# Kernel tuning notes

Hardware: AMD Instinct MI355X
Metric: run time of the kernel (lower is better)

## Reference

```python
import jax, jax.numpy as jnp
import numpy as np

D_FEATURE = 1024
HEAD = 16
D_K = 64
D_V = 64
EPS = 1e-6


def setup_inputs() -> dict:
    key = jax.random.key(0)
    ks = jax.random.split(key, 12)
    B, S = 2, 2048
    s_in = 1.0 / np.sqrt(D_FEATURE)
    s_o = 1.0 / np.sqrt(HEAD * D_V)
    return {
        "q": jax.random.normal(ks[0], (B, S, D_FEATURE), jnp.float32),
        "k": jax.random.normal(ks[1], (B, S, D_FEATURE), jnp.float32),
        "v": jax.random.normal(ks[2], (B, S, D_FEATURE), jnp.float32),
        "Wq": jax.random.uniform(ks[3], (D_FEATURE, HEAD * D_K), jnp.float32, -s_in, s_in),
        "bq": jnp.zeros((HEAD * D_K,), jnp.float32),
        "Wk": jax.random.uniform(ks[4], (D_FEATURE, HEAD * D_K), jnp.float32, -s_in, s_in),
        "bk": jnp.zeros((HEAD * D_K,), jnp.float32),
        "Wv": jax.random.uniform(ks[5], (D_FEATURE, HEAD * D_V), jnp.float32, -s_in, s_in),
        "bv": jnp.zeros((HEAD * D_V,), jnp.float32),
        "Wo": jax.random.uniform(ks[6], (HEAD * D_V, D_FEATURE), jnp.float32, -s_o, s_o),
        "bo": jnp.zeros((D_FEATURE,), jnp.float32),
        "gamma": jnp.ones((D_FEATURE,), jnp.float32),
        "beta": jnp.zeros((D_FEATURE,), jnp.float32),
    }


def reference(q, k, v, Wq, bq, Wk, bk, Wv, bv, Wo, bo, gamma, beta):
    B, Sq, _ = q.shape
    Sk, Sv = k.shape[1], v.shape[1]
    shortcut = v
    # projections -> (b, h, s, d)
    qh = (q @ Wq + bq).reshape(B, Sq, HEAD, D_K).transpose(0, 2, 1, 3)
    kh = (k @ Wk + bk).reshape(B, Sk, HEAD, D_K).transpose(0, 2, 1, 3)
    vh = (v @ Wv + bv).reshape(B, Sv, HEAD, D_V).transpose(0, 2, 1, 3)
    scale = 1.0 / np.sqrt(D_K).astype(np.float32)
    scores = jnp.einsum('bhqd,bhkd->bhqk', qh * scale, kh)
    attn = jax.nn.softmax(scores, axis=-1)  # dropout is identity (p=0 / eval)
    ctx = jnp.einsum('bhqk,bhkd->bhqd', attn, vh)
    ctx = ctx.transpose(0, 2, 1, 3).reshape(B, Sv, HEAD * D_V)
    out = ctx @ Wo + bo
    out = out + shortcut
    # LayerNorm, eps=1e-6
    mu = out.mean(-1, keepdims=True)
    var = out.var(-1, keepdims=True)
    out = (out - mu) * jax.lax.rsqrt(var + EPS) * gamma + beta
    return out
```

## Files before the change

kernel.cpp:

```cpp
#include <hip/hip_runtime.h>

#define D_FEAT 1024
#define NTOK   4096
#define SEQ    2048
#define NHEAD  16
#define DK     64
#define SPST   72
#define QSCALE 0.1803368801111204f

typedef float          f32x4 __attribute__((ext_vector_type(4)));
typedef short          s16x8 __attribute__((ext_vector_type(8)));
typedef unsigned short u16x4 __attribute__((ext_vector_type(4)));

__device__ __forceinline__ unsigned short f2bf(float f) {
  union { float f; unsigned int u; } x; x.f = f;
  unsigned int r = x.u + 0x7fffu + ((x.u >> 16) & 1u);
  return (unsigned short)(r >> 16);
}

__device__ __forceinline__ f32x4 mfma16(s16x8 a, s16x8 b, f32x4 c) {
  return __builtin_amdgcn_mfma_f32_16x16x32_bf16(a, b, c, 0, 0, 0);
}

__device__ __forceinline__ void gload16(const void* g, void* l) {
  __builtin_amdgcn_global_load_lds(
      (const __attribute__((address_space(1))) void*)g,
      (__attribute__((address_space(3))) void*)l, 16, 0, 0);
}

__global__ __launch_bounds__(256) void cast_bf16_kernel(
    const float* __restrict__ q, const float* __restrict__ k, const float* __restrict__ v,
    unsigned short* __restrict__ qb, unsigned short* __restrict__ kb, unsigned short* __restrict__ vb)
{
  int sel = blockIdx.y;
  const float* src = sel == 0 ? q : (sel == 1 ? k : v);
  unsigned short* dst = sel == 0 ? qb : (sel == 1 ? kb : vb);
  size_t i = ((size_t)blockIdx.x * 256 + threadIdx.x) * 4;
  float4 f = *(const float4*)(src + i);
  u16x4 o; o.x = f2bf(f.x); o.y = f2bf(f.y); o.z = f2bf(f.z); o.w = f2bf(f.w);
  *(u16x4*)(dst + i) = o;
}

__global__ __launch_bounds__(256) void transpose_cast_kernel(
    const float* __restrict__ W0, const float* __restrict__ W1,
    const float* __restrict__ W2, const float* __restrict__ W3,
    unsigned short* __restrict__ WT, unsigned short* __restrict__ Wot)
{
  __shared__ float tile[32][33];
  int z = blockIdx.z;
  const float* W = z == 0 ? W0 : z == 1 ? W1 : z == 2 ? W2 : W3;
  unsigned short* T = (z < 3) ? (WT + (size_t)z * 1024 * 1024) : Wot;
  int tx = threadIdx.x, ty = threadIdx.y;
  int n = blockIdx.x * 32 + tx;
  for (int i = 0; i < 4; ++i) {
    int k = blockIdx.y * 32 + ty + i * 8;
    tile[ty + i * 8][tx] = W[(size_t)k * D_FEAT + n];
  }
  __syncthreads();
  int k = blockIdx.y * 32 + tx;
  for (int i = 0; i < 4; ++i) {
    int n2 = blockIdx.x * 32 + ty + i * 8;
    T[(size_t)n2 * D_FEAT + k] = f2bf(tile[tx][ty + i * 8]);
  }
}

__global__ __launch_bounds__(256) void gemm_qkv(
    const unsigned short* __restrict__ qb, const unsigned short* __restrict__ kb,
    const unsigned short* __restrict__ vb, const unsigned short* __restrict__ WT,
    const float* __restrict__ bq, const float* __restrict__ bk, const float* __restrict__ bv,
    unsigned short* __restrict__ Qp, unsigned short* __restrict__ Kp, unsigned short* __restrict__ Vt)
{
  __shared__ __align__(16) unsigned short sA[128 * 32];
  __shared__ __align__(16) unsigned short sB[128 * 32];
  const int tid = threadIdx.x;
  const int wave = tid >> 6, lane = tid & 63;
  const int quad = lane >> 4, l16 = lane & 15;
  const int wx = wave & 1, wy = wave >> 1;
  const int bx = blockIdx.x;
  const int chunk = bx >> 3;

  const unsigned short* rA;
  const unsigned short* rB;
  int m0, n0;
  if (chunk < 2) {
    m0 = blockIdx.y * 128; n0 = (bx & 7) * 128;
    rA = (chunk ? kb : qb) + (size_t)m0 * D_FEAT;
    rB = WT + (size_t)(chunk * 1024 + n0) * D_FEAT;
  } else {
    m0 = (bx & 7) * 128; n0 = blockIdx.y * 128;
    rA = WT + (size_t)(2048 + m0) * D_FEAT;
    rB = vb + (size_t)n0 * D_FEAT;
  }

  f32x4 acc[4][4];
  for (int mt = 0; mt < 4; ++mt)
    for (int nt = 0; nt < 4; ++nt) acc[mt][nt] = (f32x4){0.f, 0.f, 0.f, 0.f};

  const int rw = lane >> 2;
  const int cl = (((lane & 3) ^ ((lane >> 3) & 3))) * 8;
  const int g0 = (quad ^ ((l16 >> 1) & 3)) * 8;

  for (int k0 = 0; k0 < D_FEAT; k0 += 32) {
    __syncthreads();
    for (int j = 0; j < 2; ++j) {
      int ch = wave * 2 + j;
      gload16(rA + (size_t)(ch * 16 + rw) * D_FEAT + k0 + cl, sA + ch * 512);
      gload16(rB + (size_t)(ch * 16 + rw) * D_FEAT + k0 + cl, sB + ch * 512);
    }
    __syncthreads();
    s16x8 af[4], bfr[4];
    for (int mt = 0; mt < 4; ++mt)
      af[mt] = *(const s16x8*)(sA + (wy * 64 + mt * 16 + l16) * 32 + g0);
    for (int nt = 0; nt < 4; ++nt)
      bfr[nt] = *(const s16x8*)(sB + (wx * 64 + nt * 16 + l16) * 32 + g0);
    for (int mt = 0; mt < 4; ++mt)
      for (int nt = 0; nt < 4; ++nt)
        acc[mt][nt] = mfma16(af[mt], bfr[nt], acc[mt][nt]);
  }

  if (chunk < 2) {
    const float* bias = chunk ? bk : bq;
    unsigned short* Cp = chunk ? Kp : Qp;
    const float scale = chunk == 0 ? QSCALE : 1.0f;
    for (int mt = 0; mt < 4; ++mt)
      for (int nt = 0; nt < 4; ++nt) {
        int col = n0 + wx * 64 + nt * 16 + l16;
        float bcol = bias[col];
        for (int r = 0; r < 4; ++r) {
          int row = m0 + wy * 64 + mt * 16 + quad * 4 + r;
          Cp[(size_t)row * D_FEAT + col] = f2bf((acc[mt][nt][r] + bcol) * scale);
        }
      }
  } else {
    for (int mt = 0; mt < 4; ++mt) {
      float bfeat[4];
      for (int r = 0; r < 4; ++r)
        bfeat[r] = bv[m0 + wy * 64 + mt * 16 + quad * 4 + r];
      for (int nt = 0; nt < 4; ++nt) {
        int n = n0 + wx * 64 + nt * 16 + l16;
        int b = n >> 11, tok = n & 2047;
        for (int r = 0; r < 4; ++r) {
          int f = m0 + wy * 64 + mt * 16 + quad * 4 + r;
          int h = f >> 6, dv = f & 63;
          Vt[(((size_t)(b * 16 + h) * 64 + dv) * SEQ) + tok] =
              f2bf(acc[mt][nt][r] + bfeat[r]);
        }
      }
    }
  }
}

__global__ __launch_bounds__(256) void gemm_o(
    const unsigned short* __restrict__ A, const unsigned short* __restrict__ Bt,
    const float* __restrict__ bias, const float* __restrict__ resid,
    float* __restrict__ Cout)
{
  __shared__ __align__(16) unsigned short sA[128 * 32];
  __shared__ __align__(16) unsigned short sB[128 * 32];
  const int tid = threadIdx.x;
  const int wave = tid >> 6, lane = tid & 63;
  const int quad = lane >> 4, l16 = lane & 15;
  const int wx = wave & 1, wy = wave >> 1;
  const int n0 = blockIdx.x * 128, m0 = blockIdx.y * 128;

  f32x4 acc[4][4];
  for (int mt = 0; mt < 4; ++mt)
    for (int nt = 0; nt < 4; ++nt) acc[mt][nt] = (f32x4){0.f, 0.f, 0.f, 0.f};

  const int rw = lane >> 2;
  const int cl = (((lane & 3) ^ ((lane >> 3) & 3))) * 8;
  const int g0 = (quad ^ ((l16 >> 1) & 3)) * 8;

  for (int k0 = 0; k0 < D_FEAT; k0 += 32) {
    __syncthreads();
    for (int j = 0; j < 2; ++j) {
      int ch = wave * 2 + j;
      gload16(A + (size_t)(m0 + ch * 16 + rw) * D_FEAT + k0 + cl, sA + ch * 512);
      gload16(Bt + (size_t)(n0 + ch * 16 + rw) * D_FEAT + k0 + cl, sB + ch * 512);
    }
    __syncthreads();
    s16x8 af[4], bfr[4];
    for (int mt = 0; mt < 4; ++mt)
      af[mt] = *(const s16x8*)(sA + (wy * 64 + mt * 16 + l16) * 32 + g0);
    for (int nt = 0; nt < 4; ++nt)
      bfr[nt] = *(const s16x8*)(sB + (wx * 64 + nt * 16 + l16) * 32 + g0);
    for (int mt = 0; mt < 4; ++mt)
      for (int nt = 0; nt < 4; ++nt)
        acc[mt][nt] = mfma16(af[mt], bfr[nt], acc[mt][nt]);
  }

  for (int mt = 0; mt < 4; ++mt)
    for (int nt = 0; nt < 4; ++nt) {
      int col = n0 + wx * 64 + nt * 16 + l16;
      float bcol = bias[col];
      for (int r = 0; r < 4; ++r) {
        int row = m0 + wy * 64 + mt * 16 + quad * 4 + r;
        Cout[(size_t)row * D_FEAT + col] =
            acc[mt][nt][r] + bcol + resid[(size_t)row * D_FEAT + col];
      }
    }
}

__global__ __launch_bounds__(256, 4) void flash_kernel(
    const unsigned short* __restrict__ Qp,
    const unsigned short* __restrict__ Kp,
    const unsigned short* __restrict__ Vt,
    unsigned short* __restrict__ ctx)
{
  __shared__ __align__(16) unsigned short sQ[64 * 64];
  __shared__ __align__(16) unsigned short sK[64 * 64];
  __shared__ __align__(16) unsigned short sV[64 * 64];
  __shared__ __align__(16) unsigned short sP[64 * SPST];

  const int tid = threadIdx.x;
  const int wave = tid >> 6, lane = tid & 63;
  const int quad = lane >> 4, l16 = lane & 15;
  const int q0 = blockIdx.x * 64;
  const int bh = blockIdx.y, b = bh >> 4, h = bh & 15;
  const size_t base = (size_t)b * SEQ * D_FEAT + (size_t)h * DK;
  const unsigned short* vt = Vt + (size_t)bh * 64 * SEQ;

  for (int i = 0; i < 2; ++i) {
    int c = tid + 256 * i;
    int row = c >> 3, csw = ((c & 7) ^ (row & 7)) * 8;
    *(s16x8*)(sQ + row * 64 + csw) =
        *(const s16x8*)(Qp + base + (size_t)(q0 + row) * D_FEAT + (c & 7) * 8);
  }
  __syncthreads();

  const int sw = l16 & 7;
  const int c0 = (quad ^ sw) * 8;
  const int c1 = ((quad + 4) ^ sw) * 8;

  const s16x8 bq0 = *(const s16x8*)(sQ + (wave * 16 + l16) * 64 + c0);
  const s16x8 bq1 = *(const s16x8*)(sQ + (wave * 16 + l16) * 64 + c1);

  s16x8 ones;
  for (int j = 0; j < 8; ++j) ones[j] = (short)0x3F80;

  float m_i = -INFINITY;
  f32x4 l_i = (f32x4){0.f, 0.f, 0.f, 0.f};
  f32x4 o[4];
  for (int nt = 0; nt < 4; ++nt) o[nt] = (f32x4){0.f, 0.f, 0.f, 0.f};

  const int rw = lane >> 3;
  const int cls = ((lane & 7) ^ (lane >> 3)) * 8;

  for (int k0 = 0; k0 < SEQ; k0 += 64) {
    __syncthreads();
    for (int j = 0; j < 2; ++j) {
      int ch = wave * 2 + j;
      gload16(Kp + base + (size_t)(k0 + ch * 8 + rw) * D_FEAT + cls, sK + ch * 512);
      gload16(vt + (size_t)(ch * 8 + rw) * SEQ + k0 + cls, sV + ch * 512);
    }
    __syncthreads();

    f32x4 st[4];
    for (int nt = 0; nt < 4; ++nt) {
      s16x8 ak0 = *(const s16x8*)(sK + (nt * 16 + l16) * 64 + c0);
      s16x8 ak1 = *(const s16x8*)(sK + (nt * 16 + l16) * 64 + c1);
      f32x4 z = (f32x4){0.f, 0.f, 0.f, 0.f};
      z = mfma16(ak0, bq0, z);
      st[nt] = mfma16(ak1, bq1, z);
    }

    float mx = st[0][0];
    for (int nt = 0; nt < 4; ++nt)
      for (int r = 0; r < 4; ++r) mx = fmaxf(mx, st[nt][r]);
    mx = fmaxf(mx, __shfl_xor(mx, 16, 64));
    mx = fmaxf(mx, __shfl_xor(mx, 32, 64));
    float mn = fmaxf(m_i, mx);
    float alpha = __builtin_exp2f(m_i - mn);
    m_i = mn;

    for (int nt = 0; nt < 4; ++nt) {
      unsigned int u[4];
      for (int r = 0; r < 4; ++r) {
        union { float f; unsigned int v; } x;
        x.f = __builtin_exp2f(st[nt][r] - mn);
        u[r] = x.v;
      }
      unsigned int w0 = __builtin_amdgcn_perm(u[1], u[0], 0x07060302u);
      unsigned int w1 = __builtin_amdgcn_perm(u[3], u[2], 0x07060302u);
      *(uint2*)(sP + (wave * 16 + l16) * SPST + nt * 16 + quad * 4) =
          make_uint2(w0, w1);
    }

    float ar[4];
    for (int r = 0; r < 4; ++r) ar[r] = __shfl(alpha, quad * 4 + r, 64);
    for (int nt = 0; nt < 4; ++nt)
      for (int r = 0; r < 4; ++r) o[nt][r] *= ar[r];
    for (int r = 0; r < 4; ++r) l_i[r] *= ar[r];

    s16x8 ap0 = *(const s16x8*)(sP + (wave * 16 + l16) * SPST + quad * 8);
    s16x8 ap1 = *(const s16x8*)(sP + (wave * 16 + l16) * SPST + 32 + quad * 8);

    f32x4 zs = (f32x4){0.f, 0.f, 0.f, 0.f};
    zs = mfma16(ap0, ones, zs);
    zs = mfma16(ap1, ones, zs);
    for (int r = 0; r < 4; ++r) l_i[r] += zs[r];

    for (int nt = 0; nt < 4; ++nt) {
      s16x8 bv0 = *(const s16x8*)(sV + (nt * 16 + l16) * 64 + c0);
      s16x8 bv1 = *(const s16x8*)(sV + (nt * 16 + l16) * 64 + c1);
      o[nt] = mfma16(ap0, bv0, o[nt]);
      o[nt] = mfma16(ap1, bv1, o[nt]);
    }
  }

  float inv[4];
  for (int r = 0; r < 4; ++r) inv[r] = __builtin_amdgcn_rcpf(l_i[r]);
  for (int nt = 0; nt < 4; ++nt)
    for (int r = 0; r < 4; ++r) {
      int row = q0 + wave * 16 + quad * 4 + r;
      ctx[base + (size_t)row * D_FEAT + nt * 16 + l16] = f2bf(o[nt][r] * inv[r]);
    }
}

__global__ __launch_bounds__(256) void ln_kernel(
    const float* __restrict__ x, const float* __restrict__ gamma,
    const float* __restrict__ beta, float* __restrict__ out)
{
  const int row = blockIdx.x, tid = threadIdx.x;
  const int wave = tid >> 6, lane = tid & 63;
  const float* xr = x + (size_t)row * D_FEAT;
  float4 v = ((const float4*)xr)[tid];
  float s  = v.x + v.y + v.z + v.w;
  float ss = v.x * v.x + v.y * v.y + v.z * v.z + v.w * v.w;
  for (int off = 1; off < 64; off <<= 1) {
    s  += __shfl_xor(s,  off, 64);
    ss += __shfl_xor(ss, off, 64);
  }
  __shared__ float red[8];
  if (lane == 0) { red[wave] = s; red[wave + 4] = ss; }
  __syncthreads();
  s  = red[0] + red[1] + red[2] + red[3];
  ss = red[4] + red[5] + red[6] + red[7];
  float mean = s * (1.f / D_FEAT);
  float var  = ss * (1.f / D_FEAT) - mean * mean;
  float rstd = rsqrtf(var + 1e-6f);
  float4 g  = ((const float4*)gamma)[tid];
  float4 bt = ((const float4*)beta)[tid];
  float4 o;
  o.x = (v.x - mean) * rstd * g.x + bt.x;
  o.y = (v.y - mean) * rstd * g.y + bt.y;
  o.z = (v.z - mean) * rstd * g.z + bt.z;
  o.w = (v.w - mean) * rstd * g.w + bt.w;
  ((float4*)(out + (size_t)row * D_FEAT))[tid] = o;
}

extern "C" void kernel_launch(void* const* d_in, const int* in_sizes, int n_in,
                              void* d_out, int out_size, void* d_ws, size_t ws_size,
                              hipStream_t stream) {
  const float* q     = (const float*)d_in[0];
  const float* k     = (const float*)d_in[1];
  const float* v     = (const float*)d_in[2];
  const float* Wq    = (const float*)d_in[3];
  const float* bq    = (const float*)d_in[4];
  const float* Wk    = (const float*)d_in[5];
  const float* bk    = (const float*)d_in[6];
  const float* Wv    = (const float*)d_in[7];
  const float* bv    = (const float*)d_in[8];
  const float* Wo    = (const float*)d_in[9];
  const float* bo    = (const float*)d_in[10];
  const float* gamma = (const float*)d_in[11];
  const float* beta  = (const float*)d_in[12];

  char* w = (char*)d_ws;
  const size_t MB = 1u << 20;
  unsigned short* qb  = (unsigned short*)(w + 0 * MB);
  unsigned short* kb  = (unsigned short*)(w + 8 * MB);
  unsigned short* vb  = (unsigned short*)(w + 16 * MB);
  unsigned short* WT  = (unsigned short*)(w + 24 * MB);
  unsigned short* Wot = (unsigned short*)(w + 30 * MB);
  unsigned short* Qp  = (unsigned short*)(w + 32 * MB);
  unsigned short* Kp  = (unsigned short*)(w + 40 * MB);
  unsigned short* Vt  = (unsigned short*)(w + 48 * MB);
  unsigned short* ctx = (unsigned short*)(w + 56 * MB);
  float*          tmp = (float*)(w + 64 * MB);

  cast_bf16_kernel<<<dim3(4096, 3), 256, 0, stream>>>(q, k, v, qb, kb, vb);
  transpose_cast_kernel<<<dim3(32, 32, 4), dim3(32, 8), 0, stream>>>(
      Wq, Wk, Wv, Wo, WT, Wot);

  gemm_qkv<<<dim3(24, 32), 256, 0, stream>>>(qb, kb, vb, WT, bq, bk, bv, Qp, Kp, Vt);

  flash_kernel<<<dim3(SEQ / 64, 32), 256, 0, stream>>>(Qp, Kp, Vt, ctx);

  gemm_o<<<dim3(8, 32), 256, 0, stream>>>(ctx, Wot, bo, v, tmp);

  ln_kernel<<<NTOK, 256, 0, stream>>>(tmp, gamma, beta, (float*)d_out);
}
```

Baseline: 280.5 us.

## Rewrite flash attention with 32x32 MFMA and 128-row query tiles; shrink gemm_o N tile

The flash kernel now uses 32x32x16 bf16 MFMA with each wave owning 32 query rows. Blocks cover 128 queries, so each K/V tile is shared by twice as many rows, and P is staged in the Q shared buffer. Row sums are computed with adds and one shuffle instead of a ones-MFMA, which removes the separate P buffer and the extra MFMA. gemm_o tile width drops to 64 columns so the launch has twice as many blocks and better CU fill. The cost is more registers per thread and fewer blocks per CU for flash (launch bounds 2), plus half the flash grid size.

```diff
diff --git a/kernel.cpp b/kernel.cpp
--- a/kernel.cpp
+++ b/kernel.cpp
@@ -5,12 +5,12 @@
 #define SEQ    2048
 #define NHEAD  16
 #define DK     64
-#define SPST   72
 #define QSCALE 0.1803368801111204f
 
-typedef float          f32x4 __attribute__((ext_vector_type(4)));
-typedef short          s16x8 __attribute__((ext_vector_type(8)));
-typedef unsigned short u16x4 __attribute__((ext_vector_type(4)));
+typedef float          f32x4  __attribute__((ext_vector_type(4)));
+typedef float          f32x16 __attribute__((ext_vector_type(16)));
+typedef short          s16x8  __attribute__((ext_vector_type(8)));
+typedef unsigned short u16x4  __attribute__((ext_vector_type(4)));
 
 __device__ __forceinline__ unsigned short f2bf(float f) {
   union { float f; unsigned int u; } x; x.f = f;
@@ -20,6 +20,9 @@
 
 __device__ __forceinline__ f32x4 mfma16(s16x8 a, s16x8 b, f32x4 c) {
   return __builtin_amdgcn_mfma_f32_16x16x32_bf16(a, b, c, 0, 0, 0);
+}
+__device__ __forceinline__ f32x16 mfma32(s16x8 a, s16x8 b, f32x16 c) {
+  return __builtin_amdgcn_mfma_f32_32x32x16_bf16(a, b, c, 0, 0, 0);
 }
 
 __device__ __forceinline__ void gload16(const void* g, void* l) {
@@ -156,16 +159,16 @@
     float* __restrict__ Cout)
 {
   __shared__ __align__(16) unsigned short sA[128 * 32];
-  __shared__ __align__(16) unsigned short sB[128 * 32];
+  __shared__ __align__(16) unsigned short sB[64 * 32];
   const int tid = threadIdx.x;
   const int wave = tid >> 6, lane = tid & 63;
   const int quad = lane >> 4, l16 = lane & 15;
   const int wx = wave & 1, wy = wave >> 1;
-  const int n0 = blockIdx.x * 128, m0 = blockIdx.y * 128;
-
-  f32x4 acc[4][4];
+  const int n0 = blockIdx.x * 64, m0 = blockIdx.y * 128;
+
+  f32x4 acc[4][2];
   for (int mt = 0; mt < 4; ++mt)
-    for (int nt = 0; nt < 4; ++nt) acc[mt][nt] = (f32x4){0.f, 0.f, 0.f, 0.f};
+    for (int nt = 0; nt < 2; ++nt) acc[mt][nt] = (f32x4){0.f, 0.f, 0.f, 0.f};
 
   const int rw = lane >> 2;
   const int cl = (((lane & 3) ^ ((lane >> 3) & 3))) * 8;
@@ -176,22 +179,22 @@
     for (int j = 0; j < 2; ++j) {
       int ch = wave * 2 + j;
       gload16(A + (size_t)(m0 + ch * 16 + rw) * D_FEAT + k0 + cl, sA + ch * 512);
-      gload16(Bt + (size_t)(n0 + ch * 16 + rw) * D_FEAT + k0 + cl, sB + ch * 512);
-    }
-    __syncthreads();
-    s16x8 af[4], bfr[4];
+    }
+    gload16(Bt + (size_t)(n0 + wave * 16 + rw) * D_FEAT + k0 + cl, sB + wave * 512);
+    __syncthreads();
+    s16x8 af[4], bfr[2];
     for (int mt = 0; mt < 4; ++mt)
       af[mt] = *(const s16x8*)(sA + (wy * 64 + mt * 16 + l16) * 32 + g0);
-    for (int nt = 0; nt < 4; ++nt)
-      bfr[nt] = *(const s16x8*)(sB + (wx * 64 + nt * 16 + l16) * 32 + g0);
+    for (int nt = 0; nt < 2; ++nt)
+      bfr[nt] = *(const s16x8*)(sB + (wx * 32 + nt * 16 + l16) * 32 + g0);
     for (int mt = 0; mt < 4; ++mt)
-      for (int nt = 0; nt < 4; ++nt)
+      for (int nt = 0; nt < 2; ++nt)
         acc[mt][nt] = mfma16(af[mt], bfr[nt], acc[mt][nt]);
   }
 
   for (int mt = 0; mt < 4; ++mt)
-    for (int nt = 0; nt < 4; ++nt) {
-      int col = n0 + wx * 64 + nt * 16 + l16;
+    for (int nt = 0; nt < 2; ++nt) {
+      int col = n0 + wx * 32 + nt * 16 + l16;
       float bcol = bias[col];
       for (int r = 0; r < 4; ++r) {
         int row = m0 + wy * 64 + mt * 16 + quad * 4 + r;
@@ -201,120 +204,127 @@
     }
 }
 
-__global__ __launch_bounds__(256, 4) void flash_kernel(
+__global__ __launch_bounds__(256, 2) void flash_kernel(
     const unsigned short* __restrict__ Qp,
     const unsigned short* __restrict__ Kp,
     const unsigned short* __restrict__ Vt,
     unsigned short* __restrict__ ctx)
 {
-  __shared__ __align__(16) unsigned short sQ[64 * 64];
+  __shared__ __align__(16) unsigned short sQ[128 * 64];
   __shared__ __align__(16) unsigned short sK[64 * 64];
   __shared__ __align__(16) unsigned short sV[64 * 64];
-  __shared__ __align__(16) unsigned short sP[64 * SPST];
 
   const int tid = threadIdx.x;
   const int wave = tid >> 6, lane = tid & 63;
-  const int quad = lane >> 4, l16 = lane & 15;
-  const int q0 = blockIdx.x * 64;
-  const int bh = blockIdx.y, b = bh >> 4, h = bh & 15;
-  const size_t base = (size_t)b * SEQ * D_FEAT + (size_t)h * DK;
+  const int l32 = lane & 31, h = lane >> 5;
+  const int q0 = blockIdx.x * 128;
+  const int bh = blockIdx.y, b = bh >> 4, hd = bh & 15;
+  const size_t base = (size_t)b * SEQ * D_FEAT + (size_t)hd * DK;
   const unsigned short* vt = Vt + (size_t)bh * 64 * SEQ;
 
-  for (int i = 0; i < 2; ++i) {
-    int c = tid + 256 * i;
-    int row = c >> 3, csw = ((c & 7) ^ (row & 7)) * 8;
-    *(s16x8*)(sQ + row * 64 + csw) =
-        *(const s16x8*)(Qp + base + (size_t)(q0 + row) * D_FEAT + (c & 7) * 8);
+  const int rw8 = lane >> 3;
+  const int cls = ((lane & 7) ^ (lane >> 3)) * 8;
+
+  for (int j = 0; j < 4; ++j) {
+    int ch = wave * 4 + j;
+    gload16(Qp + base + (size_t)(q0 + ch * 8 + rw8) * D_FEAT + cls, sQ + ch * 512);
   }
   __syncthreads();
 
-  const int sw = l16 & 7;
-  const int c0 = (quad ^ sw) * 8;
-  const int c1 = ((quad + 4) ^ sw) * 8;
-
-  const s16x8 bq0 = *(const s16x8*)(sQ + (wave * 16 + l16) * 64 + c0);
-  const s16x8 bq1 = *(const s16x8*)(sQ + (wave * 16 + l16) * 64 + c1);
-
-  s16x8 ones;
-  for (int j = 0; j < 8; ++j) ones[j] = (short)0x3F80;
-
-  float m_i = -INFINITY;
-  f32x4 l_i = (f32x4){0.f, 0.f, 0.f, 0.f};
-  f32x4 o[4];
-  for (int nt = 0; nt < 4; ++nt) o[nt] = (f32x4){0.f, 0.f, 0.f, 0.f};
-
-  const int rw = lane >> 3;
-  const int cls = ((lane & 7) ^ (lane >> 3)) * 8;
+  const int qrow = wave * 32 + l32;
+  const int qsw = qrow & 7;
+  s16x8 bq[4];
+  for (int s = 0; s < 4; ++s)
+    bq[s] = *(const s16x8*)(sQ + qrow * 64 + ((2 * s + h) ^ qsw) * 8);
+
+  unsigned short* sP = sQ;
+
+  f32x16 o0, o1;
+  for (int r = 0; r < 16; ++r) { o0[r] = 0.f; o1[r] = 0.f; }
+  float m_i = -INFINITY, l_i = 0.f;
+
+  const int ksw0 = l32 & 7;
 
   for (int k0 = 0; k0 < SEQ; k0 += 64) {
     __syncthreads();
     for (int j = 0; j < 2; ++j) {
       int ch = wave * 2 + j;
-      gload16(Kp + base + (size_t)(k0 + ch * 8 + rw) * D_FEAT + cls, sK + ch * 512);
-      gload16(vt + (size_t)(ch * 8 + rw) * SEQ + k0 + cls, sV + ch * 512);
-    }
-    __syncthreads();
-
-    f32x4 st[4];
-    for (int nt = 0; nt < 4; ++nt) {
-      s16x8 ak0 = *(const s16x8*)(sK + (nt * 16 + l16) * 64 + c0);
-      s16x8 ak1 = *(const s16x8*)(sK + (nt * 16 + l16) * 64 + c1);
-      f32x4 z = (f32x4){0.f, 0.f, 0.f, 0.f};
-      z = mfma16(ak0, bq0, z);
-      st[nt] = mfma16(ak1, bq1, z);
-    }
-
-    float mx = st[0][0];
-    for (int nt = 0; nt < 4; ++nt)
-      for (int r = 0; r < 4; ++r) mx = fmaxf(mx, st[nt][r]);
-    mx = fmaxf(mx, __shfl_xor(mx, 16, 64));
+      gload16(Kp + base + (size_t)(k0 + ch * 8 + rw8) * D_FEAT + cls, sK + ch * 512);
+      gload16(vt + (size_t)(ch * 8 + rw8) * SEQ + k0 + cls, sV + ch * 512);
+    }
+    __syncthreads();
+
+    f32x16 st0, st1;
+    for (int r = 0; r < 16; ++r) { st0[r] = 0.f; st1[r] = 0.f; }
+    for (int s = 0; s < 4; ++s) {
+      int csw = ((2 * s + h) ^ ksw0) * 8;
+      s16x8 a0 = *(const s16x8*)(sK + l32 * 64 + csw);
+      s16x8 a1 = *(const s16x8*)(sK + (32 + l32) * 64 + csw);
+      st0 = mfma32(a0, bq[s], st0);
+      st1 = mfma32(a1, bq[s], st1);
+    }
+
+    float mx = st0[0];
+    for (int r = 0; r < 16; ++r) { mx = fmaxf(mx, st0[r]); mx = fmaxf(mx, st1[r]); }
     mx = fmaxf(mx, __shfl_xor(mx, 32, 64));
     float mn = fmaxf(m_i, mx);
     float alpha = __builtin_exp2f(m_i - mn);
     m_i = mn;
 
-    for (int nt = 0; nt < 4; ++nt) {
+    float sum = 0.f;
+    const int rowb = qrow * 64;
+    for (int g = 0; g < 4; ++g) {
       unsigned int u[4];
       for (int r = 0; r < 4; ++r) {
         union { float f; unsigned int v; } x;
-        x.f = __builtin_exp2f(st[nt][r] - mn);
-        u[r] = x.v;
+        x.f = __builtin_exp2f(st0[4 * g + r] - mn);
+        sum += x.f; u[r] = x.v;
       }
       unsigned int w0 = __builtin_amdgcn_perm(u[1], u[0], 0x07060302u);
       unsigned int w1 = __builtin_amdgcn_perm(u[3], u[2], 0x07060302u);
-      *(uint2*)(sP + (wave * 16 + l16) * SPST + nt * 16 + quad * 4) =
-          make_uint2(w0, w1);
-    }
-
-    float ar[4];
-    for (int r = 0; r < 4; ++r) ar[r] = __shfl(alpha, quad * 4 + r, 64);
-    for (int nt = 0; nt < 4; ++nt)
-      for (int r = 0; r < 4; ++r) o[nt][r] *= ar[r];
-    for (int r = 0; r < 4; ++r) l_i[r] *= ar[r];
-
-    s16x8 ap0 = *(const s16x8*)(sP + (wave * 16 + l16) * SPST + quad * 8);
-    s16x8 ap1 = *(const s16x8*)(sP + (wave * 16 + l16) * SPST + 32 + quad * 8);
-
-    f32x4 zs = (f32x4){0.f, 0.f, 0.f, 0.f};
-    zs = mfma16(ap0, ones, zs);
-    zs = mfma16(ap1, ones, zs);
-    for (int r = 0; r < 4; ++r) l_i[r] += zs[r];
-
-    for (int nt = 0; nt < 4; ++nt) {
-      s16x8 bv0 = *(const s16x8*)(sV + (nt * 16 + l16) * 64 + c0);
-      s16x8 bv1 = *(const s16x8*)(sV + (nt * 16 + l16) * 64 + c1);
-      o[nt] = mfma16(ap0, bv0, o[nt]);
-      o[nt] = mfma16(ap1, bv1, o[nt]);
-    }
-  }
-
-  float inv[4];
-  for (int r = 0; r < 4; ++r) inv[r] = __builtin_amdgcn_rcpf(l_i[r]);
-  for (int nt = 0; nt < 4; ++nt)
-    for (int r = 0; r < 4; ++r) {
-      int row = q0 + wave * 16 + quad * 4 + r;
-      ctx[base + (size_t)row * D_FEAT + nt * 16 + l16] = f2bf(o[nt][r] * inv[r]);
-    }
+      *(uint2*)(sP + rowb + ((g ^ qsw) * 8) + 4 * h) = make_uint2(w0, w1);
+    }
+    for (int g = 0; g < 4; ++g) {
+      unsigned int u[4];
+      for (int r = 0; r < 4; ++r) {
+        union { float f; unsigned int v; } x;
+        x.f = __builtin_exp2f(st1[4 * g + r] - mn);
+        sum += x.f; u[r] = x.v;
+      }
+      unsigned int w0 = __builtin_amdgcn_perm(u[1], u[0], 0x07060302u);
+      unsigned int w1 = __builtin_amdgcn_perm(u[3], u[2], 0x07060302u);
+      *(uint2*)(sP + rowb + (((4 + g) ^ qsw) * 8) + 4 * h) = make_uint2(w0, w1);
+    }
+    sum += __shfl_xor(sum, 32, 64);
+    l_i = l_i * alpha + sum;
+
+    for (int r = 0; r < 16; ++r) { o0[r] *= alpha; o1[r] *= alpha; }
+
+    s16x8 bp[4];
+    for (int s = 0; s < 4; ++s)
+      bp[s] = *(const s16x8*)(sP + rowb + ((2 * s + h) ^ qsw) * 8);
+
+    for (int s = 0; s < 4; ++s) {
+      int csw = ((2 * s + h) ^ ksw0) * 8;
+      s16x8 a0 = *(const s16x8*)(sV + l32 * 64 + csw);
+      s16x8 a1 = *(const s16x8*)(sV + (32 + l32) * 64 + csw);
+      o0 = mfma32(a0, bp[s], o0);
+      o1 = mfma32(a1, bp[s], o1);
+    }
+  }
+
+  float inv = __builtin_amdgcn_rcpf(l_i);
+  unsigned short* crow = ctx + base + (size_t)(q0 + qrow) * D_FEAT;
+  for (int g = 0; g < 4; ++g) {
+    u16x4 ov;
+    for (int r = 0; r < 4; ++r) ov[r] = f2bf(o0[4 * g + r] * inv);
+    *(u16x4*)(crow + 8 * g + 4 * h) = ov;
+  }
+  for (int g = 0; g < 4; ++g) {
+    u16x4 ov;
+    for (int r = 0; r < 4; ++r) ov[r] = f2bf(o1[4 * g + r] * inv);
+    *(u16x4*)(crow + 32 + 8 * g + 4 * h) = ov;
+  }
 }
 
 __global__ __launch_bounds__(256) void ln_kernel(
@@ -385,9 +395,9 @@
 
   gemm_qkv<<<dim3(24, 32), 256, 0, stream>>>(qb, kb, vb, WT, bq, bk, bv, Qp, Kp, Vt);
 
-  flash_kernel<<<dim3(SEQ / 64, 32), 256, 0, stream>>>(Qp, Kp, Vt, ctx);
-
-  gemm_o<<<dim3(8, 32), 256, 0, stream>>>(ctx, Wot, bo, v, tmp);
+  flash_kernel<<<dim3(SEQ / 128, 32), 256, 0, stream>>>(Qp, Kp, Vt, ctx);
+
+  gemm_o<<<dim3(16, 32), 256, 0, stream>>>(ctx, Wot, bo, v, tmp);
 
   ln_kernel<<<NTOK, 256, 0, stream>>>(tmp, gamma, beta, (float*)d_out);
 }
```

Result: no change. 278.4 us (-0.7%).
